# Kernel tuning notes

Hardware: AMD Instinct MI355X
Metric: run time of the kernel (lower is better)

## Reference

```python
import jax, jax.numpy as jnp
import numpy as np


def setup_inputs() -> dict:
    key = jax.random.key(0)
    k1, = jax.random.split(key, 1)
    B, T = 2048, 4096
    inputs = jax.random.uniform(k1, (B, T, 3), dtype=jnp.float32)
    # learned scalar params (init 0.5 as in torch module)
    x1 = jnp.float32(0.5)
    x2 = jnp.float32(0.5)
    x3 = jnp.float32(0.5)
    # unit-hydrograph conv weights: normalized exponential decay, kernel=30
    i = jnp.arange(30, dtype=jnp.float32)
    uh1_w = jnp.exp(-i / 5.0)
    uh1_w = (uh1_w / uh1_w.sum()).reshape(1, 1, 30)
    uh2_w = jnp.exp(-i / 10.0)
    uh2_w = (uh2_w / uh2_w.sum()).reshape(1, 1, 30)
    return {"inputs": inputs, "x1": x1, "x2": x2, "x3": x3,
            "uh1_w": uh1_w, "uh2_w": uh2_w}


def _same_conv1d(x, w):
    # x: [B, 1, T]; w: [1, 1, 30]. torch padding='same' for k=30 pads (14, 15).
    return jax.lax.conv_general_dilated(
        x, w, window_strides=(1,), padding=[(14, 15)],
        dimension_numbers=("NCH", "OIH", "NCH"))


def _gr4j_forward(inputs, x1, x2, x3, uh1_w, uh2_w):
    inputs = inputs.astype(jnp.float32)
    p = inputs[:, :, 0]      # [B, T] precipitation
    t = inputs[:, :, 1]      # [B, T] temperature
    dayl = inputs[:, :, 2]   # [B, T] daylength
    pet = 29.8 * (dayl * 24.0) * 0.611 * jnp.exp(17.3 * t / (t + 237.3)) / (t + 273.2)

    B, T = p.shape
    X1 = jnp.clip(x1, 1.0 / 2000.0, 1.0) * 2000.0
    X2 = x2 * 40.0 - 20.0
    X3 = jnp.clip(x3, 1.0 / 300.0, 1.0) * 300.0
    # torch uses float(X1)/float(X3) for clamp bounds -> detached constants
    X1d = jax.lax.stop_gradient(X1)
    X3d = jax.lax.stop_gradient(X3)

    s0 = jnp.full((B,), 0.3, jnp.float32) * X1
    r0 = jnp.full((B,), 0.7, jnp.float32) * X3

    def step(carry, xs):
        s, r = carry
        P, E = xs  # each [B]
        cond = P >= E
        Pn = jnp.where(cond, P - E, 0.0)
        En = jnp.where(cond, 0.0, E - P)
        th_p = jnp.tanh(Pn / X1)
        Ps = jnp.where(cond,
                       X1 * (1.0 - (s / X1) ** 2) * th_p / (1.0 + (s / X1) * th_p),
                       0.0)
        th_e = jnp.tanh(En / X1)
        Es = jnp.where(~cond,
                       s * (2.0 - s / X1) * th_e / (1.0 + (1.0 - s / X1) * th_e),
                       0.0)
        s = jnp.clip(s + Ps - Es, 0.0, X1d)
        Perc = s * (1.0 - (1.0 + ((4.0 / 9.0) * s / X1) ** 4) ** (-0.25))
        s = jnp.clip(s - Perc, 0.0, X1d)
        PR = Perc + (Pn - Ps)
        Fx = X2 * (r / X3) ** 3.5
        r = jnp.maximum(r + Fx, 0.0)
        Qr = r * (1.0 - (1.0 + (r / X3) ** 4) ** (-0.25))
        r = jnp.clip(r - Qr, 0.0, X3d)
        return (s, r), (PR, Qr)

    # scan over time: xs are [T, B]
    (_, _), (PR_seq, Qr_seq) = jax.lax.scan(step, (s0, r0), (p.T, pet.T))
    PR = PR_seq.T  # [B, T]
    Qt = Qr_seq.T  # [B, T]

    uh1_contrib = _same_conv1d((0.9 * PR)[:, None, :], uh1_w)[:, 0, :]
    uh2_contrib = _same_conv1d((0.1 * PR)[:, None, :], uh2_w)[:, 0, :]
    q_sim = Qt + uh1_contrib + uh2_contrib
    return q_sim[:, :, None]  # [B, T, 1]


def reference(inputs, x1, x2, x3, uh1_w, uh2_w):
    return _gr4j_forward(inputs, x1, x2, x3, uh1_w, uh2_w)
```

## Files before the change

### kernel.cpp

```cpp
#include <hip/hip_runtime.h>

#define BB 2048
#define TT 4096
#define TQ (TT / 4)
#define K1C 0.00975461f

typedef __attribute__((ext_vector_type(4))) _Float16 half4;

#define HOLD2(U) asm volatile("" : "+v"((U).x), "+v"((U).y))
#define HOLD4(V) asm volatile("" : "+v"((V).x), "+v"((V).y), "+v"((V).z), "+v"((V).w))

__global__ __launch_bounds__(256) void precompute_kernel(
    const float* __restrict__ inp, const float* __restrict__ x1p,
    const float* __restrict__ x2p, const float* __restrict__ x3p,
    half4* __restrict__ wTh, half4* __restrict__ sumsh,
    float* __restrict__ qr) {

    if (blockIdx.x == 0) {
        float X2 = x2p[0] * 40.0f - 20.0f;
        float X3 = fminf(fmaxf(x3p[0], 1.0f / 300.0f), 1.0f) * 300.0f;
        if (X2 == 0.0f) {
            float rn0 = 0.7f;
            float rn2 = rn0 * rn0;
            float u0  = 1.0f / (rn2 * rn2);
#pragma unroll
            for (int i = 0; i < 16; ++i) {
                int t = threadIdx.x + 256 * i;
                float v  = u0 + (float)t;
                float q  = __builtin_amdgcn_rcpf(v);
                float h  = fmaf(q, fmaf(q, fmaf(q, -0.09521484f,
                                  0.1171875f), -0.15625f), 0.25f);
                float w  = q * h;
                float rn = __builtin_amdgcn_rsqf(sqrtf(v));
                qr[t] = (X3 * rn) * w;
            }
        } else if (threadIdx.x == 0) {
            float invX3 = 1.0f / X3;
            float r = 0.7f * X3;
            for (int t = 0; t < TT; ++t) {
                float rx  = r * invX3;
                float rx3 = rx * rx * rx;
                float pw  = rx3 * sqrtf(rx);
                float r1  = fmaxf(fmaf(X2, pw, r), 0.0f);
                float m   = r1 * invX3;
                float m2  = m * m;
                float z   = fmaf(m2, m2, 1.0f);
                float u   = __builtin_amdgcn_rsqf(sqrtf(z));
                float Qr  = r1 * (1.0f - u);
                r = fminf(r1 * u, X3);
                qr[t] = Qr;
            }
        }
        return;
    }

    __shared__ _Float16 ldsh[64 * 68];
    const int bid = blockIdx.x - 1;
    const int tiles_t = TT / 64;
    const int t0 = (bid % tiles_t) * 64;
    const int b0 = (bid / tiles_t) * 64;
    const float X1 = fminf(fmaxf(x1p[0], 1.0f / 2000.0f), 1.0f) * 2000.0f;
    const float invX1 = 1.0f / X1;

    const int q  = threadIdx.x & 15;
    const int r  = threadIdx.x >> 4;
    float4 L[12];
#pragma unroll
    for (int i = 0; i < 4; ++i) {
        int bl = r + 16 * i;
        size_t e = ((size_t)(b0 + bl) * TT + (t0 + 4 * q)) * 3;
        const float4* src = reinterpret_cast<const float4*>(inp + e);
        L[3 * i + 0] = src[0];
        L[3 * i + 1] = src[1];
        L[3 * i + 2] = src[2];
    }
    __builtin_amdgcn_sched_barrier(0);
#pragma unroll
    for (int i = 0; i < 4; ++i) {
        int bl = r + 16 * i;
        HOLD4(L[3 * i + 0]); HOLD4(L[3 * i + 1]); HOLD4(L[3 * i + 2]);
        float4 A4 = L[3 * i + 0], B4 = L[3 * i + 1], C4 = L[3 * i + 2];
        float pk[4], tk[4], dk[4];
        pk[0] = A4.x; tk[0] = A4.y; dk[0] = A4.z;
        pk[1] = A4.w; tk[1] = B4.x; dk[1] = B4.y;
        pk[2] = B4.z; tk[2] = B4.w; dk[2] = C4.x;
        pk[3] = C4.y; tk[3] = C4.z; dk[3] = C4.w;
        half4 hw;
#pragma unroll
        for (int j = 0; j < 4; ++j) {
            float tt = tk[j];
            float u1 = __builtin_amdgcn_rcpf(tt + 237.3f);
            float u2 = __builtin_amdgcn_rcpf(tt + 273.2f);
            float ex = exp2f((24.9586242f * tt) * u1);
            float pet = (436.9872f * dk[j]) * (ex * u2);
            float w = (pk[j] - pet) * invX1;
            if (j == 0) hw.x = (_Float16)w; else if (j == 1) hw.y = (_Float16)w;
            else if (j == 2) hw.z = (_Float16)w; else hw.w = (_Float16)w;
        }
        *reinterpret_cast<half4*>(&ldsh[bl * 68 + 4 * q]) = hw;
    }
    __syncthreads();

    const int tl = threadIdx.x & 63;
    const int r4 = threadIdx.x >> 6;
    const int tq0 = t0 >> 2;
    for (int i = 0; i < 4; ++i) {
        int tr = i * 4 + r4;
        half4 hv = *reinterpret_cast<const half4*>(&ldsh[tl * 68 + tr * 4]);
        wTh[(size_t)(tq0 + tr) * BB + (b0 + tl)] = hv;
    }
#pragma unroll
    for (int i = 0; i < 2; ++i) {
        int job = threadIdx.x + 256 * i;
        int bl = job & 63, g = job >> 6;
        half4 ha = *reinterpret_cast<const half4*>(&ldsh[bl * 68 + g * 8]);
        half4 hb = *reinterpret_cast<const half4*>(&ldsh[bl * 68 + g * 8 + 4]);
        float s1 = 0.f, s2 = 0.f, s3 = 0.f, s4 = 0.f;
#pragma unroll
        for (int j = 0; j < 8; ++j) {
            float w = (j < 4) ? (float)((j == 0) ? ha.x : (j == 1) ? ha.y :
                                        (j == 2) ? ha.z : ha.w)
                              : (float)((j == 4) ? hb.x : (j == 5) ? hb.y :
                                        (j == 6) ? hb.z : hb.w);
            float a = fabsf(w);
            s1 += w; s2 += a; s3 += w * a; s4 += w * w;
        }
        half4 sh;
        sh.x = (_Float16)s1; sh.y = (_Float16)s2;
        sh.z = (_Float16)(s3 * 512.0f);
        sh.w = (_Float16)(s4 * 512.0f);
        sumsh[(size_t)((t0 >> 3) + g) * BB + (b0 + bl)] = sh;
    }
}

#define PSTEP(W, D)                                                          \
    {                                                                        \
        float w_  = (W);                                                     \
        float aw_ = __builtin_fabsf(w_);                                     \
        float ub_ = aw_ * bm;                                                \
        float Gw_ = fmaf(w_, cc, -ub_);                                      \
        float q_  = bm * w_;                                                 \
        float tt_ = fmaf(0.5f, aw_, q_);                                     \
        D = fmaf(-Gw_, tt_, Gw_);                                            \
    }

__global__ __launch_bounds__(64) void pilot_kernel(
    const uint2* __restrict__ sumsh, float* __restrict__ snap) {

    const int b = blockIdx.x * 64 + threadIdx.x;
    float Z = 0.3f;
    const uint2* __restrict__ sp = sumsh + b;

    uint2 A[16], B[16], C[16], D[16];

#define PLOAD(BUF, SET)                                                      \
    _Pragma("unroll")                                                        \
    for (int k = 0; k < 16; ++k)                                             \
        BUF[k] = sp[(size_t)((SET) * 16 + k) * BB];

#define HOLDBUF(BUF)                                                         \
    _Pragma("unroll")                                                        \
    for (int k = 0; k < 16; ++k) HOLD2(BUF[k]);

#define PMACRO(U)                                                            \
    {                                                                        \
        uint2 u_ = (U);                                                      \
        half4 h_ = __builtin_bit_cast(half4, u_);                            \
        float s1 = (float)h_.x, s2 = (float)h_.y;                            \
        float s3 = (float)h_.z * 0.001953125f;                               \
        float s4 = (float)h_.w * 0.001953125f;                               \
        float bm = Z - 0.5f;                                                 \
        float cc = fmaf(-bm, bm, 0.75f);                                     \
        float bm2 = bm * bm;                                                 \
        float z2 = Z * Z, z4 = z2 * z2;                                      \
        float pn = (z4 * Z) * K1C;                                           \
        float A_ = fmaf(cc, s1, -(bm * s2));                                 \
        float w1 = fmaf(-0.5f, cc, bm2);                                     \
        float T3 = w1 * s3;                                                  \
        float c2 = cc - 0.5f;                                                \
        float cb = c2 * bm;                                                  \
        float T4 = cb * s4;                                                  \
        float dd = (A_ + T3) - T4;                                           \
        float base = fmaf(pn, -8.0f, Z);                                     \
        Z = base + dd;                                                       \
    }

#define PSET(BUF, J)                                                         \
    {                                                                        \
        HOLDBUF(BUF);                                                        \
        PMACRO(BUF[0]);  PMACRO(BUF[1]);  PMACRO(BUF[2]);  PMACRO(BUF[3]);   \
        PMACRO(BUF[4]);  PMACRO(BUF[5]);  PMACRO(BUF[6]);  PMACRO(BUF[7]);   \
        PMACRO(BUF[8]);  PMACRO(BUF[9]);  PMACRO(BUF[10]); PMACRO(BUF[11]);  \
        PMACRO(BUF[12]); PMACRO(BUF[13]);                                    \
        snap[(size_t)(J) * BB + b] = Z;                                      \
        PMACRO(BUF[14]); PMACRO(BUF[15]);                                    \
    }

    PLOAD(A, 0); PLOAD(B, 1);
    for (int k = 0; k < 7; ++k) {
        int i = 4 * k;
        PLOAD(C, i + 2); __builtin_amdgcn_sched_barrier(0); PSET(A, i);
        PLOAD(D, i + 3); __builtin_amdgcn_sched_barrier(0); PSET(B, i + 1);
        PLOAD(A, i + 4); __builtin_amdgcn_sched_barrier(0); PSET(C, i + 2);
        PLOAD(B, i + 5); __builtin_amdgcn_sched_barrier(0); PSET(D, i + 3);
    }
    PLOAD(C, 30); __builtin_amdgcn_sched_barrier(0);
    PSET(A, 28); PSET(B, 29); PSET(C, 30);

#undef PSET
#undef PMACRO
#undef HOLDBUF
#undef PLOAD
}

__global__ __launch_bounds__(64) void seg_kernel(
    const uint2* __restrict__ wTh, const float* __restrict__ snap,
    const float* __restrict__ qr, const float* __restrict__ uh1,
    const float* __restrict__ uh2, const float* __restrict__ x1p,
    float* __restrict__ outp) {
    __shared__ float tile[64 * 65];
    const int lane = threadIdx.x;
    const int sig = blockIdx.x >> 5;
    const int b0 = (blockIdx.x & 31) * 64;
    const int b = b0 + lane;
    const int T0 = sig << 7;
    const float X1 = fminf(fmaxf(x1p[0], 1.0f / 2000.0f), 1.0f) * 2000.0f;

    float WX[30];
#pragma unroll
    for (int k = 0; k < 30; ++k)
        WX[k] = X1 * fmaf(0.9f, uh1[k], 0.1f * uh2[k]);

    float Z = 0.3f;
    if (sig > 0) Z = snap[(size_t)(sig - 1) * BB + b];
    float zs0 = Z * Z, z40 = zs0 * zs0;
    float pn0 = (z40 * Z) * K1C;
    float pnL1 = pn0, pnL2 = pn0, pnL3 = pn0, pnL4 = pn0;

    float ring[32];
#pragma unroll
    for (int i = 0; i < 32; ++i) ring[i] = 0.0f;

    const int R0 = 32 * sig - 4;
    const uint2* __restrict__ vp = wTh + b;
    uint2 A[8], B[8];

#define LOADC(BUF, C)                                                        \
    _Pragma("unroll")                                                        \
    for (int k = 0; k < 8; ++k) {                                            \
        int rq = R0 + 8 * (C) + k;                                           \
        BUF[k] = (rq >= 0 && rq < TQ) ? vp[(size_t)rq * BB]                  \
                                      : make_uint2(0u, 0u);                  \
    }

#define HOLDC(BUF)                                                           \
    _Pragma("unroll")                                                        \
    for (int k = 0; k < 8; ++k) HOLD2(BUF[k]);

#define EMIT(C, MM, I)                                                       \
    {                                                                        \
        float acc = 0.0f;                                                    \
        _Pragma("unroll")                                                    \
        for (int k = 0; k < 30; ++k)                                         \
            acc = fmaf(WX[k], ring[(4 * (MM) + (I) + 3 + k) & 31], acc);     \
        tile[((32 * (C) + 4 * (MM) + (I) - 15) & 63) * 65 + lane] = acc;     \
    }

#define SMACRO(U4, MM, C)                                                    \
    {                                                                        \
        uint2 u4_ = (U4);                                                    \
        half4 h4_ = __builtin_bit_cast(half4, u4_);                          \
        float4 v4;                                                           \
        v4.x = (float)h4_.x; v4.y = (float)h4_.y;                            \
        v4.z = (float)h4_.z; v4.w = (float)h4_.w;                            \
        float bm = Z - 0.5f;                                                 \
        float cc = fmaf(-bm, bm, 0.75f);                                     \
        float L12 = pnL1 + pnL2, L123 = L12 + pnL3, L1234 = L123 + pnL4;     \
        float e1 = Z - pnL1, e2 = Z - L12, e3 = Z - L123, e4 = Z - L1234;    \
        float d1, d2, d3, d4;                                                \
        PSTEP(v4.x, d1); PSTEP(v4.y, d2); PSTEP(v4.z, d3); PSTEP(v4.w, d4);  \
        float p2 = d1 + d2, t34 = d3 + d4;                                   \
        float p3 = p2 + d3, p4 = p2 + t34;                                   \
        float z1 = Z + d1, z2 = e1 + p2, z3 = e2 + p3, z4 = e3 + p4;         \
        Z = e4 + p4;                                                         \
        float a1 = z1 * z1, a2 = z2 * z2, a3 = z3 * z3, a4 = z4 * z4;        \
        float g1 = a1 * a1, g2 = a2 * a2, g3 = a3 * a3, g4 = a4 * a4;        \
        float h1 = z1 * K1C, h2 = z2 * K1C, h3 = z3 * K1C, h4 = z4 * K1C;    \
        float n1 = g1 * h1, n2 = g2 * h2, n3 = g3 * h3, n4 = g4 * h4;        \
        float pr1 = fmaxf(v4.x - d1, 0.0f) + n1;                             \
        float pr2 = fmaxf(v4.y - d2, 0.0f) + n2;                             \
        float pr3 = fmaxf(v4.z - d3, 0.0f) + n3;                             \
        float pr4 = fmaxf(v4.w - d4, 0.0f) + n4;                             \
        pnL1 = n1; pnL2 = n2; pnL3 = n3; pnL4 = n4;                          \
        int tb_ = T0 - 16 + 32 * (C) + 4 * (MM);                             \
        pr1 = ((unsigned)(tb_ + 0) < (unsigned)TT) ? pr1 : 0.0f;             \
        pr2 = ((unsigned)(tb_ + 1) < (unsigned)TT) ? pr2 : 0.0f;             \
        pr3 = ((unsigned)(tb_ + 2) < (unsigned)TT) ? pr3 : 0.0f;             \
        pr4 = ((unsigned)(tb_ + 3) < (unsigned)TT) ? pr4 : 0.0f;             \
        ring[(4 * (MM) + 0) & 31] = pr1;                                     \
        ring[(4 * (MM) + 1) & 31] = pr2;                                     \
        ring[(4 * (MM) + 2) & 31] = pr3;                                     \
        ring[(4 * (MM) + 3) & 31] = pr4;                                     \
        EMIT(C, MM, 0); EMIT(C, MM, 1); EMIT(C, MM, 2); EMIT(C, MM, 3);      \
    }

#define COMPUTE(BUF, C)                                                      \
    HOLDC(BUF);                                                              \
    SMACRO(BUF[0], 0, C); SMACRO(BUF[1], 1, C);                              \
    SMACRO(BUF[2], 2, C); SMACRO(BUF[3], 3, C);                              \
    SMACRO(BUF[4], 4, C); SMACRO(BUF[5], 5, C);                              \
    SMACRO(BUF[6], 6, C); SMACRO(BUF[7], 7, C);

#define FLUSH(J, RLO, RHI)                                                   \
    {                                                                        \
        int tb = T0 - 16 + 32 * (J);                                         \
        int RB = 32 * ((J) & 1);                                             \
        int a4 = (lane & 7) * 4;                                             \
        int tq = tb + a4;                                                    \
        int tqc = min(max(tq, 0), TT - 4);                                   \
        float4 q4 = *reinterpret_cast<const float4*>(qr + tqc);              \
        bool ok = (a4 >= (RLO)) && (a4 < (RHI));                             \
        _Pragma("unroll")                                                    \
        for (int r2 = 0; r2 < 8; ++r2) {                                     \
            int bl = (lane >> 3) + 8 * r2;                                   \
            float v0 = tile[(RB + a4 + 0) * 65 + bl];                        \
            float v1 = tile[(RB + a4 + 1) * 65 + bl];                        \
            float v2 = tile[(RB + a4 + 2) * 65 + bl];                        \
            float v3 = tile[(RB + a4 + 3) * 65 + bl];                        \
            if (ok) {                                                        \
                float4 o = make_float4(q4.x + v0, q4.y + v1,                 \
                                       q4.z + v2, q4.w + v3);                \
                *reinterpret_cast<float4*>(                                  \
                    outp + (size_t)(b0 + bl) * TT + tq) = o;                 \
            }                                                                \
        }                                                                    \
    }

    LOADC(A, 0); LOADC(B, 1);
    __builtin_amdgcn_sched_barrier(0);
    COMPUTE(A, 0);
    LOADC(A, 2);
    __builtin_amdgcn_sched_barrier(0);
    COMPUTE(B, 1);
    __syncthreads(); FLUSH(0, 16, 32);
    LOADC(B, 3);
    __builtin_amdgcn_sched_barrier(0);
    COMPUTE(A, 2);
    __syncthreads(); FLUSH(1, 0, 32);
    LOADC(A, 4);
    __builtin_amdgcn_sched_barrier(0);
    COMPUTE(B, 3);
    __syncthreads(); FLUSH(2, 0, 32);
    COMPUTE(A, 4);
    __syncthreads(); FLUSH(3, 0, 32); FLUSH(4, 0, 16);

#undef FLUSH
#undef COMPUTE
#undef SMACRO
#undef EMIT
#undef HOLDC
#undef LOADC
}

extern "C" void kernel_launch(void* const* d_in, const int* in_sizes, int n_in,
                              void* d_out, int out_size, void* d_ws, size_t ws_size,
                              hipStream_t stream) {
    const float* inp = (const float*)d_in[0];
    const float* x1  = (const float*)d_in[1];
    const float* x2  = (const float*)d_in[2];
    const float* x3  = (const float*)d_in[3];
    const float* uh1 = (const float*)d_in[4];
    const float* uh2 = (const float*)d_in[5];
    float* out = (float*)d_out;

    char* ws = (char*)d_ws;
    half4* wTh   = (half4*)ws;
    half4* sumsh = (half4*)(ws + (size_t)TQ * BB * 8);
    float* qrp   = (float*)(ws + (size_t)TQ * BB * 8 + (size_t)512 * BB * 8);
    float* snap  = qrp + TT;

    precompute_kernel<<<(TT / 64) * (BB / 64) + 1, 256, 0, stream>>>(
        inp, x1, x2, x3, wTh, sumsh, qrp);
    pilot_kernel<<<32, 64, 0, stream>>>((const uint2*)sumsh, snap);
    seg_kernel<<<1024, 64, 0, stream>>>((const uint2*)wTh, snap, qrp,
                                        uh1, uh2, x1, out);
}
```

Measured before the change: 78.91 us.

## Halve seg_kernel segment length and pack two wavefronts per block

The pilot kernel now writes state snapshots every 64 timesteps instead of every 128, and also processes the final buffer. seg_kernel jobs then cover 64-step segments, with two independent 64-lane jobs per 128-thread block, each using its own LDS tile. The aim is twice as many parallel segment jobs with shorter serial chains in the segment pass. In exchange, more snapshot stores and more redundant warm-up/halo work per output, and extra syncthreads shared across the two waves.

Result: faster. 75.42 us (-4.4%).

```diff
diff --git a/kernel.cpp b/kernel.cpp
--- a/kernel.cpp
+++ b/kernel.cpp
@@ -62,8 +62,8 @@
     const float X1 = fminf(fmaxf(x1p[0], 1.0f / 2000.0f), 1.0f) * 2000.0f;
     const float invX1 = 1.0f / X1;
 
-    const int q  = threadIdx.x & 15;
-    const int r  = threadIdx.x >> 4;
+    const int q = threadIdx.x & 15;
+    const int r = threadIdx.x >> 4;
     float4 L[12];
 #pragma unroll
     for (int i = 0; i < 4; ++i) {
@@ -188,11 +188,12 @@
 #define PSET(BUF, J)                                                         \
     {                                                                        \
         HOLDBUF(BUF);                                                        \
-        PMACRO(BUF[0]);  PMACRO(BUF[1]);  PMACRO(BUF[2]);  PMACRO(BUF[3]);   \
-        PMACRO(BUF[4]);  PMACRO(BUF[5]);  PMACRO(BUF[6]);  PMACRO(BUF[7]);   \
-        PMACRO(BUF[8]);  PMACRO(BUF[9]);  PMACRO(BUF[10]); PMACRO(BUF[11]);  \
-        PMACRO(BUF[12]); PMACRO(BUF[13]);                                    \
-        snap[(size_t)(J) * BB + b] = Z;                                      \
+        PMACRO(BUF[0]);  PMACRO(BUF[1]);  PMACRO(BUF[2]);                    \
+        PMACRO(BUF[3]);  PMACRO(BUF[4]);  PMACRO(BUF[5]);                    \
+        snap[(size_t)(2 * (J)) * BB + b] = Z;                                \
+        PMACRO(BUF[6]);  PMACRO(BUF[7]);  PMACRO(BUF[8]);  PMACRO(BUF[9]);   \
+        PMACRO(BUF[10]); PMACRO(BUF[11]); PMACRO(BUF[12]); PMACRO(BUF[13]);  \
+        snap[(size_t)(2 * (J) + 1) * BB + b] = Z;                            \
         PMACRO(BUF[14]); PMACRO(BUF[15]);                                    \
     }
 
@@ -204,8 +205,9 @@
         PLOAD(A, i + 4); __builtin_amdgcn_sched_barrier(0); PSET(C, i + 2);
         PLOAD(B, i + 5); __builtin_amdgcn_sched_barrier(0); PSET(D, i + 3);
     }
-    PLOAD(C, 30); __builtin_amdgcn_sched_barrier(0);
-    PSET(A, 28); PSET(B, 29); PSET(C, 30);
+    PLOAD(C, 30); __builtin_amdgcn_sched_barrier(0); PSET(A, 28);
+    PLOAD(D, 31); __builtin_amdgcn_sched_barrier(0); PSET(B, 29);
+    PSET(C, 30); PSET(D, 31);
 
 #undef PSET
 #undef PMACRO
@@ -213,17 +215,20 @@
 #undef PLOAD
 }
 
-__global__ __launch_bounds__(64) void seg_kernel(
+__global__ __launch_bounds__(128) void seg_kernel(
     const uint2* __restrict__ wTh, const float* __restrict__ snap,
     const float* __restrict__ qr, const float* __restrict__ uh1,
     const float* __restrict__ uh2, const float* __restrict__ x1p,
     float* __restrict__ outp) {
-    __shared__ float tile[64 * 65];
-    const int lane = threadIdx.x;
-    const int sig = blockIdx.x >> 5;
-    const int b0 = (blockIdx.x & 31) * 64;
-    const int b = b0 + lane;
-    const int T0 = sig << 7;
+    __shared__ float tile2[2][64 * 65];
+    const int wid  = threadIdx.x >> 6;
+    const int lane = threadIdx.x & 63;
+    float* tile_ = tile2[wid];
+    const int job = (blockIdx.x << 1) | wid;
+    const int sig = job >> 5;
+    const int b0  = (job & 31) * 64;
+    const int b   = b0 + lane;
+    const int T0  = sig << 6;
     const float X1 = fminf(fmaxf(x1p[0], 1.0f / 2000.0f), 1.0f) * 2000.0f;
 
     float WX[30];
@@ -241,7 +246,7 @@
 #pragma unroll
     for (int i = 0; i < 32; ++i) ring[i] = 0.0f;
 
-    const int R0 = 32 * sig - 4;
+    const int R0 = 16 * sig - 4;
     const uint2* __restrict__ vp = wTh + b;
     uint2 A[8], B[8];
 
@@ -263,7 +268,7 @@
         _Pragma("unroll")                                                    \
         for (int k = 0; k < 30; ++k)                                         \
             acc = fmaf(WX[k], ring[(4 * (MM) + (I) + 3 + k) & 31], acc);     \
-        tile[((32 * (C) + 4 * (MM) + (I) - 15) & 63) * 65 + lane] = acc;     \
+        tile_[((32 * (C) + 4 * (MM) + (I) - 15) & 63) * 65 + lane] = acc;    \
     }
 
 #define SMACRO(U4, MM, C)                                                    \
@@ -323,10 +328,10 @@
         _Pragma("unroll")                                                    \
         for (int r2 = 0; r2 < 8; ++r2) {                                     \
             int bl = (lane >> 3) + 8 * r2;                                   \
-            float v0 = tile[(RB + a4 + 0) * 65 + bl];                        \
-            float v1 = tile[(RB + a4 + 1) * 65 + bl];                        \
-            float v2 = tile[(RB + a4 + 2) * 65 + bl];                        \
-            float v3 = tile[(RB + a4 + 3) * 65 + bl];                        \
+            float v0 = tile_[(RB + a4 + 0) * 65 + bl];                       \
+            float v1 = tile_[(RB + a4 + 1) * 65 + bl];                       \
+            float v2 = tile_[(RB + a4 + 2) * 65 + bl];                       \
+            float v3 = tile_[(RB + a4 + 3) * 65 + bl];                       \
             if (ok) {                                                        \
                 float4 o = make_float4(q4.x + v0, q4.y + v1,                 \
                                        q4.z + v2, q4.w + v3);                \
@@ -343,16 +348,9 @@
     __builtin_amdgcn_sched_barrier(0);
     COMPUTE(B, 1);
     __syncthreads(); FLUSH(0, 16, 32);
-    LOADC(B, 3);
-    __builtin_amdgcn_sched_barrier(0);
+    __syncthreads();
     COMPUTE(A, 2);
-    __syncthreads(); FLUSH(1, 0, 32);
-    LOADC(A, 4);
-    __builtin_amdgcn_sched_barrier(0);
-    COMPUTE(B, 3);
-    __syncthreads(); FLUSH(2, 0, 32);
-    COMPUTE(A, 4);
-    __syncthreads(); FLUSH(3, 0, 32); FLUSH(4, 0, 16);
+    __syncthreads(); FLUSH(1, 0, 32); FLUSH(2, 0, 16);
 
 #undef FLUSH
 #undef COMPUTE
@@ -382,6 +380,6 @@
     precompute_kernel<<<(TT / 64) * (BB / 64) + 1, 256, 0, stream>>>(
         inp, x1, x2, x3, wTh, sumsh, qrp);
     pilot_kernel<<<32, 64, 0, stream>>>((const uint2*)sumsh, snap);
-    seg_kernel<<<1024, 64, 0, stream>>>((const uint2*)wTh, snap, qrp,
-                                        uh1, uh2, x1, out);
+    seg_kernel<<<1024, 128, 0, stream>>>((const uint2*)wTh, snap, qrp,
+                                         uh1, uh2, x1, out);
 }
```
